# Performance work log

Hardware: AMD Instinct MI355X
Metric: run time of the kernel (lower is better)

Reference implementation:

```python
import jax, jax.numpy as jnp
import numpy as np

N = 40000      # nodes
E = 640000     # edges (avg degree 16)
D = 128        # feature dim (in_features == all hidden_dims due to residual)


def setup_inputs() -> dict:
    key = jax.random.key(0)
    ks = jax.random.split(key, 8)
    xavier = (6.0 / (D + D)) ** 0.5
    return {
        "x": jax.random.normal(ks[0], (N, D), dtype=jnp.float32),
        "edge_index": jax.random.randint(ks[1], (2, E), 0, N, dtype=jnp.int64),
        "W_t": jax.random.uniform(ks[2], (D, D), jnp.float32, -xavier, xavier),
        "b_t": jnp.zeros((D,), jnp.float32),
        "W0": jax.random.uniform(ks[3], (D, D), jnp.float32, -xavier, xavier),
        "b0": jnp.zeros((D,), jnp.float32),
        "W1": jax.random.uniform(ks[4], (D, D), jnp.float32, -xavier, xavier),
        "b1": jnp.zeros((D,), jnp.float32),
    }


def _gcn_layer(h, row, col, W, b):
    # linear transform, then edge-wise gather + scatter-add aggregation
    z = jnp.matmul(h, W)                                  # [N, D]
    agg = jnp.zeros_like(z).at[row].add(z[col])           # out[row] += z[col]
    return jax.nn.relu(agg + b)


def reference(x, edge_index, W_t, b_t, W0, b0, W1, b1):
    row, col = edge_index[0], edge_index[1]
    h = jnp.matmul(x, W_t) + b_t                          # self.transform
    # residual GCN layers (dropout p=0.0 -> identity; eval mode)
    h = h + _gcn_layer(h, row, col, W0, b0)
    h = h + _gcn_layer(h, row, col, W1, b1)
    return h
```

## Files before the change

### kernel.cpp

```cpp
#include <hip/hip_runtime.h>
#include <hip/hip_bf16.h>

#define N_NODES 40000
#define N_EDGES 640000
#define DIM     128
#define NB      157
#define GEMMB   625
#define HEB     1250

typedef __attribute__((ext_vector_type(8))) short short8;
typedef __attribute__((ext_vector_type(4))) float f32x4;

__device__ inline short f2bf(float f) {
    __hip_bfloat16 h = __float2bfloat16(f);
    return *reinterpret_cast<short*>(&h);
}
__device__ inline float bf2f(short u) {
    union { unsigned int i; float f; } x;
    x.i = ((unsigned int)(unsigned short)u) << 16;
    return x.f;
}

__device__ inline int fragidx(int k, int n) {
    int kb = k >> 5, kq = (k >> 3) & 3, j = k & 7;
    int nt = n >> 4, nl = n & 15;
    return (((kb * 8 + nt) * 64 + kq * 16 + nl) * 8 + j);
}

__global__ __launch_bounds__(256) void prep_zero(const float* __restrict__ Wt,
                                                 const float* __restrict__ W0,
                                                 const float* __restrict__ W1,
                                                 const float* __restrict__ bt,
                                                 short* __restrict__ WtF,
                                                 short* __restrict__ WfF,
                                                 short* __restrict__ W1F,
                                                 float* __restrict__ btf,
                                                 int* __restrict__ counts,
                                                 int* __restrict__ flagtot) {
    int b = blockIdx.x;
    if (b < 64) {
        int gid = b * 256 + threadIdx.x;
        int k = gid >> 7, n = gid & 127;
        float wf = 0.f;
        for (int kk = 0; kk < 128; ++kk)
            wf += Wt[k * 128 + kk] * W0[kk * 128 + n];
        int fi = fragidx(k, n);
        WtF[fi] = f2bf(Wt[k * 128 + n]);
        W1F[fi] = f2bf(W1[k * 128 + n]);
        WfF[fi] = f2bf(wf);
        if (gid < 128) {
            float s = 0.f;
            for (int kk = 0; kk < 128; ++kk) s += bt[kk] * W0[kk * 128 + n];
            btf[n] = s;
        }
    } else if (b < 64 + NB) {
        int i = (b - 64) * 256 + threadIdx.x;
        if (i < N_NODES) counts[i] = 0;
    } else {
        flagtot[threadIdx.x]       = 0;
        flagtot[threadIdx.x + 256] = 0;
    }
}

__global__ __launch_bounds__(256) void histrank_gemm(const int* __restrict__ rows,
                                                     int* __restrict__ counts,
                                                     unsigned short* __restrict__ rank,
                                                     const float* __restrict__ A,
                                                     const short* __restrict__ WtF,
                                                     const short* __restrict__ WfF,
                                                     const float* __restrict__ bt,
                                                     const float* __restrict__ btf,
                                                     float* __restrict__ H,
                                                     __hip_bfloat16* __restrict__ Z) {
    if (blockIdx.x < HEB) {
        int gid = blockIdx.x * 256 + threadIdx.x;
#pragma unroll
        for (int h = 0; h < 2; ++h) {
            int e = gid + h * HEB * 256;
            int r = rows[e];
            rank[e] = (unsigned short)atomicAdd(&counts[r], 1);
        }
        return;
    }

    const int t    = threadIdx.x;
    const int wave = t >> 6;
    const int l    = t & 63;
    const int nl   = l & 15;
    const int quad = l >> 4;
    const int wRow = (blockIdx.x - HEB) * 64 + wave * 16;

    f32x4 accH[8], accZ[8];
#pragma unroll
    for (int nt = 0; nt < 8; ++nt) {
        accH[nt] = (f32x4){0.f, 0.f, 0.f, 0.f};
        accZ[nt] = (f32x4){0.f, 0.f, 0.f, 0.f};
    }

#pragma unroll
    for (int kb = 0; kb < 4; ++kb) {
        const float* ap = A + (size_t)(wRow + nl) * 128 + kb * 32 + quad * 8;
        float4 f0 = *(const float4*)ap;
        float4 f1 = *(const float4*)(ap + 4);
        short8 afrag;
        afrag[0] = f2bf(f0.x); afrag[1] = f2bf(f0.y);
        afrag[2] = f2bf(f0.z); afrag[3] = f2bf(f0.w);
        afrag[4] = f2bf(f1.x); afrag[5] = f2bf(f1.y);
        afrag[6] = f2bf(f1.z); afrag[7] = f2bf(f1.w);
#pragma unroll
        for (int nt = 0; nt < 8; ++nt) {
            int off = ((kb * 8 + nt) * 64 + l) * 8;
            short8 bt_frag = *(const short8*)&WtF[off];
            short8 bf_frag = *(const short8*)&WfF[off];
            accH[nt] = __builtin_amdgcn_mfma_f32_16x16x32_bf16(afrag, bt_frag, accH[nt], 0, 0, 0);
            accZ[nt] = __builtin_amdgcn_mfma_f32_16x16x32_bf16(afrag, bf_frag, accZ[nt], 0, 0, 0);
        }
    }

#pragma unroll
    for (int nt = 0; nt < 8; ++nt) {
        int col = nt * 16 + nl;
        float bH = bt[col];
        float bZ = btf[col];
#pragma unroll
        for (int r = 0; r < 4; ++r) {
            int row = wRow + quad * 4 + r;
            H[(size_t)row * 128 + col] = accH[nt][r] + bH;
            *(short*)&Z[(size_t)row * 128 + col] = f2bf(accZ[nt][r] + bZ);
        }
    }
}

__global__ __launch_bounds__(256) void scan_onepass(const int* __restrict__ counts,
                                                    int* __restrict__ flags,
                                                    int* __restrict__ totals,
                                                    int* __restrict__ row_ptr) {
    __shared__ int sh[256];
    const int b = blockIdx.x;
    const int t = threadIdx.x;
    const int i = b * 256 + t;

    int c = (i < N_NODES) ? counts[i] : 0;
    int val = c;
    sh[t] = val;
    __syncthreads();
    for (int off = 1; off < 256; off <<= 1) {
        int a = (t >= off) ? sh[t - off] : 0;
        __syncthreads();
        val += a;
        sh[t] = val;
        __syncthreads();
    }
    const int excl  = val - c;
    const int total = sh[255];

    if (t == 0) {
        atomicExch(&totals[b], total);
        __threadfence();
        atomicExch(&flags[b], 1);
    }

    int v = 0;
    if (t < NB) {
        while (atomicAdd(&flags[t], 0) == 0) { }
        v = atomicAdd(&totals[t], 0);
    }
    __syncthreads();
    int val2 = v;
    sh[t] = val2;
    __syncthreads();
    for (int off = 1; off < 256; off <<= 1) {
        int a = (t >= off) ? sh[t - off] : 0;
        __syncthreads();
        val2 += a;
        sh[t] = val2;
        __syncthreads();
    }
    int blkOff = (b == 0) ? 0 : sh[b - 1];

    if (i < N_NODES) row_ptr[i] = excl + blkOff;
    if (i == 0) row_ptr[N_NODES] = N_EDGES;
}

__global__ __launch_bounds__(256) void scatter_plain(const int* __restrict__ rows,
                                                     const int* __restrict__ cols,
                                                     const unsigned short* __restrict__ rank,
                                                     const int* __restrict__ row_ptr,
                                                     unsigned short* __restrict__ adj) {
    int gid = blockIdx.x * 256 + threadIdx.x;
#pragma unroll
    for (int h = 0; h < 2; ++h) {
        int e = gid + h * HEB * 256;
        int r = rows[e];
        adj[row_ptr[r] + (int)rank[e]] = (unsigned short)cols[e];
    }
}

__global__ __launch_bounds__(256) void agg0_gemm(const __hip_bfloat16* __restrict__ z0,
                                                 const int* __restrict__ row_ptr,
                                                 const unsigned short* __restrict__ adj,
                                                 const float* __restrict__ bias,
                                                 const short* __restrict__ W1F,
                                                 float* __restrict__ H,
                                                 __hip_bfloat16* __restrict__ Z1) {
    __shared__ short hs[16][136];

    const int t    = threadIdx.x;
    const int wave = t >> 6;
    const int l    = t & 63;
    const int quad = l >> 4;
    const int sl   = l & 15;
    const int nodeBase = blockIdx.x * 16;

#pragma unroll
    for (int u = 0; u < 4; ++u) {
        const int m    = wave * 4 + u;
        const int node = nodeBase + m;
        const int s = row_ptr[node];
        const int e = row_ptr[node + 1];

        float acc[8];
#pragma unroll
        for (int j = 0; j < 8; ++j) acc[j] = 0.f;

        int it = s + quad;
        for (; it + 12 < e; it += 16) {
            int c0 = adj[it];
            int c1 = adj[it + 4];
            int c2 = adj[it + 8];
            int c3 = adj[it + 12];
            short8 v0 = *(const short8*)&z0[(size_t)c0 * DIM + sl * 8];
            short8 v1 = *(const short8*)&z0[(size_t)c1 * DIM + sl * 8];
            short8 v2 = *(const short8*)&z0[(size_t)c2 * DIM + sl * 8];
            short8 v3 = *(const short8*)&z0[(size_t)c3 * DIM + sl * 8];
#pragma unroll
            for (int j = 0; j < 8; ++j)
                acc[j] += (bf2f(v0[j]) + bf2f(v1[j])) + (bf2f(v2[j]) + bf2f(v3[j]));
        }
        for (; it + 4 < e; it += 8) {
            int c0 = adj[it];
            int c1 = adj[it + 4];
            short8 v0 = *(const short8*)&z0[(size_t)c0 * DIM + sl * 8];
            short8 v1 = *(const short8*)&z0[(size_t)c1 * DIM + sl * 8];
#pragma unroll
            for (int j = 0; j < 8; ++j) acc[j] += bf2f(v0[j]) + bf2f(v1[j]);
        }
        if (it < e) {
            int c = adj[it];
            short8 v = *(const short8*)&z0[(size_t)c * DIM + sl * 8];
#pragma unroll
            for (int j = 0; j < 8; ++j) acc[j] += bf2f(v[j]);
        }

#pragma unroll
        for (int j = 0; j < 8; ++j) acc[j] += __shfl_xor(acc[j], 16, 64);
#pragma unroll
        for (int j = 0; j < 8; ++j) acc[j] += __shfl_xor(acc[j], 32, 64);

        if (quad == 0) {
            float* hp = H + (size_t)node * DIM + sl * 8;
            float4 h0 = *(float4*)hp;
            float4 h1 = *(float4*)(hp + 4);
            float4 b0v = *(const float4*)&bias[sl * 8];
            float4 b1v = *(const float4*)&bias[sl * 8 + 4];
            float r[8];
            r[0] = acc[0] + b0v.x; r[1] = acc[1] + b0v.y; r[2] = acc[2] + b0v.z; r[3] = acc[3] + b0v.w;
            r[4] = acc[4] + b1v.x; r[5] = acc[5] + b1v.y; r[6] = acc[6] + b1v.z; r[7] = acc[7] + b1v.w;
            float hn[8];
            hn[0] = h0.x; hn[1] = h0.y; hn[2] = h0.z; hn[3] = h0.w;
            hn[4] = h1.x; hn[5] = h1.y; hn[6] = h1.z; hn[7] = h1.w;
            short8 o;
#pragma unroll
            for (int j = 0; j < 8; ++j) {
                float rr = r[j] > 0.f ? r[j] : 0.f;
                hn[j] += rr;
                o[j] = f2bf(hn[j]);
            }
            *(float4*)hp       = make_float4(hn[0], hn[1], hn[2], hn[3]);
            *(float4*)(hp + 4) = make_float4(hn[4], hn[5], hn[6], hn[7]);
            *(short8*)&hs[m][sl * 8] = o;
        }
    }
    __syncthreads();

    f32x4 acc2[2];
    acc2[0] = (f32x4){0.f, 0.f, 0.f, 0.f};
    acc2[1] = (f32x4){0.f, 0.f, 0.f, 0.f};
#pragma unroll
    for (int kb = 0; kb < 4; ++kb) {
        short8 afrag = *(const short8*)&hs[sl][kb * 32 + quad * 8];
#pragma unroll
        for (int nt2 = 0; nt2 < 2; ++nt2) {
            int nt = wave * 2 + nt2;
            short8 bfrag = *(const short8*)&W1F[((kb * 8 + nt) * 64 + l) * 8];
            acc2[nt2] = __builtin_amdgcn_mfma_f32_16x16x32_bf16(afrag, bfrag, acc2[nt2], 0, 0, 0);
        }
    }
#pragma unroll
    for (int nt2 = 0; nt2 < 2; ++nt2) {
        int col = (wave * 2 + nt2) * 16 + sl;
#pragma unroll
        for (int r = 0; r < 4; ++r) {
            int row = nodeBase + quad * 4 + r;
            *(short*)&Z1[(size_t)row * 128 + col] = f2bf(acc2[nt2][r]);
        }
    }
}

__global__ __launch_bounds__(256) void agg_final(const __hip_bfloat16* __restrict__ z,
                                                 const int* __restrict__ row_ptr,
                                                 const unsigned short* __restrict__ adj,
                                                 const float* __restrict__ bias,
                                                 float* __restrict__ H) {
    const int wave = threadIdx.x >> 6;
    const int l    = threadIdx.x & 63;
    const int quad = l >> 4;
    const int sl   = l & 15;
    const int node = blockIdx.x * 4 + wave;
    if (node >= N_NODES) return;

    const int s = row_ptr[node];
    const int e = row_ptr[node + 1];

    float acc[8];
#pragma unroll
    for (int j = 0; j < 8; ++j) acc[j] = 0.f;

    int it = s + quad;
    for (; it + 12 < e; it += 16) {
        int c0 = adj[it];
        int c1 = adj[it + 4];
        int c2 = adj[it + 8];
        int c3 = adj[it + 12];
        short8 v0 = *(const short8*)&z[(size_t)c0 * DIM + sl * 8];
        short8 v1 = *(const short8*)&z[(size_t)c1 * DIM + sl * 8];
        short8 v2 = *(const short8*)&z[(size_t)c2 * DIM + sl * 8];
        short8 v3 = *(const short8*)&z[(size_t)c3 * DIM + sl * 8];
#pragma unroll
        for (int j = 0; j < 8; ++j)
            acc[j] += (bf2f(v0[j]) + bf2f(v1[j])) + (bf2f(v2[j]) + bf2f(v3[j]));
    }
    for (; it + 4 < e; it += 8) {
        int c0 = adj[it];
        int c1 = adj[it + 4];
        short8 v0 = *(const short8*)&z[(size_t)c0 * DIM + sl * 8];
        short8 v1 = *(const short8*)&z[(size_t)c1 * DIM + sl * 8];
#pragma unroll
        for (int j = 0; j < 8; ++j) acc[j] += bf2f(v0[j]) + bf2f(v1[j]);
    }
    if (it < e) {
        int c = adj[it];
        short8 v = *(const short8*)&z[(size_t)c * DIM + sl * 8];
#pragma unroll
        for (int j = 0; j < 8; ++j) acc[j] += bf2f(v[j]);
    }

#pragma unroll
    for (int j = 0; j < 8; ++j) acc[j] += __shfl_xor(acc[j], 16, 64);
#pragma unroll
    for (int j = 0; j < 8; ++j) acc[j] += __shfl_xor(acc[j], 32, 64);

    if (quad == 0) {
        float* hp = H + (size_t)node * DIM + sl * 8;
        float4 h0 = *(float4*)hp;
        float4 h1 = *(float4*)(hp + 4);
        float4 b0 = *(const float4*)&bias[sl * 8];
        float4 b1 = *(const float4*)&bias[sl * 8 + 4];
        float r0 = acc[0] + b0.x, r1 = acc[1] + b0.y, r2 = acc[2] + b0.z, r3 = acc[3] + b0.w;
        float r4 = acc[4] + b1.x, r5 = acc[5] + b1.y, r6 = acc[6] + b1.z, r7 = acc[7] + b1.w;
        h0.x += r0 > 0.f ? r0 : 0.f;  h0.y += r1 > 0.f ? r1 : 0.f;
        h0.z += r2 > 0.f ? r2 : 0.f;  h0.w += r3 > 0.f ? r3 : 0.f;
        h1.x += r4 > 0.f ? r4 : 0.f;  h1.y += r5 > 0.f ? r5 : 0.f;
        h1.z += r6 > 0.f ? r6 : 0.f;  h1.w += r7 > 0.f ? r7 : 0.f;
        *(float4*)hp       = h0;
        *(float4*)(hp + 4) = h1;
    }
}

extern "C" void kernel_launch(void* const* d_in, const int* in_sizes, int n_in,
                              void* d_out, int out_size, void* d_ws, size_t ws_size,
                              hipStream_t stream) {
    const float* x   = (const float*)d_in[0];
    const int*   ei  = (const int*)d_in[1];
    const float* W_t = (const float*)d_in[2];
    const float* b_t = (const float*)d_in[3];
    const float* W0  = (const float*)d_in[4];
    const float* b0  = (const float*)d_in[5];
    const float* W1  = (const float*)d_in[6];
    const float* b1  = (const float*)d_in[7];

    const int* rows = ei;
    const int* cols = ei + N_EDGES;

    float* H = (float*)d_out;

    char* w = (char*)d_ws;
    __hip_bfloat16* Z0 = (__hip_bfloat16*)w;  w += (size_t)N_NODES * DIM * 2;
    __hip_bfloat16* Z1 = (__hip_bfloat16*)w;  w += (size_t)N_NODES * DIM * 2;
    short* WtF = (short*)w;  w += 128 * 128 * 2;
    short* WfF = (short*)w;  w += 128 * 128 * 2;
    short* W1F = (short*)w;  w += 128 * 128 * 2;
    float* btf = (float*)w;  w += 128 * 4;
    int* row_ptr = (int*)w;  w += (N_NODES + 1) * 4;
    int* counts  = (int*)w;  w += N_NODES * 4;
    int* flags   = (int*)w;  w += 256 * 4;
    int* totals  = (int*)w;  w += 256 * 4;
    unsigned short* rank = (unsigned short*)w;  w += (size_t)N_EDGES * 2;
    unsigned short* adj  = (unsigned short*)w;

    const int aggBlocks = (N_NODES + 3) / 4;

    prep_zero<<<64 + NB + 1, 256, 0, stream>>>(W_t, W0, W1, b_t, WtF, WfF, W1F,
                                               btf, counts, flags);

    histrank_gemm<<<HEB + GEMMB, 256, 0, stream>>>(rows, counts, rank,
                                                   x, WtF, WfF, b_t, btf, H, Z0);

    scan_onepass<<<NB, 256, 0, stream>>>(counts, flags, totals, row_ptr);

    scatter_plain<<<HEB, 256, 0, stream>>>(rows, cols, rank, row_ptr, adj);

    agg0_gemm<<<N_NODES / 16, 256, 0, stream>>>(Z0, row_ptr, adj, b0, W1F, H, Z1);

    agg_final<<<aggBlocks, 256, 0, stream>>>(Z1, row_ptr, adj, b1, H);
}
```

Measured before the change: 204.5 us.

## Replicate degree counters four ways and store second-layer features as fp8

The degree histogram is spread over four replicated counter arrays chosen by block index, which cuts atomic contention on hot rows. The scan sums the four copies and writes a per-replica absolute offset that the scatter uses. The second GCN layer's transformed features Z1 move from bf16 to fp8 (e4m3 via the packed conversion builtins), halving the bytes gathered in the final aggregation. The fp8 storage loses precision on activations and may break tolerance, and the replicas add extra zeroing and offset traffic.

```diff
diff --git a/kernel.cpp b/kernel.cpp
--- a/kernel.cpp
+++ b/kernel.cpp
@@ -7,9 +7,11 @@
 #define NB      157
 #define GEMMB   625
 #define HEB     1250
+#define NREP    4
 
 typedef __attribute__((ext_vector_type(8))) short short8;
 typedef __attribute__((ext_vector_type(4))) float f32x4;
+typedef __attribute__((ext_vector_type(2))) float f32x2;
 
 __device__ inline short f2bf(float f) {
     __hip_bfloat16 h = __float2bfloat16(f);
@@ -35,7 +37,7 @@
                                                  short* __restrict__ WfF,
                                                  short* __restrict__ W1F,
                                                  float* __restrict__ btf,
-                                                 int* __restrict__ counts,
+                                                 int* __restrict__ counts4,
                                                  int* __restrict__ flagtot) {
     int b = blockIdx.x;
     if (b < 64) {
@@ -53,9 +55,9 @@
             for (int kk = 0; kk < 128; ++kk) s += bt[kk] * W0[kk * 128 + n];
             btf[n] = s;
         }
-    } else if (b < 64 + NB) {
+    } else if (b < 64 + NREP * NB) {
         int i = (b - 64) * 256 + threadIdx.x;
-        if (i < N_NODES) counts[i] = 0;
+        if (i < NREP * N_NODES) counts4[i] = 0;
     } else {
         flagtot[threadIdx.x]       = 0;
         flagtot[threadIdx.x + 256] = 0;
@@ -63,7 +65,7 @@
 }
 
 __global__ __launch_bounds__(256) void histrank_gemm(const int* __restrict__ rows,
-                                                     int* __restrict__ counts,
+                                                     int* __restrict__ counts4,
                                                      unsigned short* __restrict__ rank,
                                                      const float* __restrict__ A,
                                                      const short* __restrict__ WtF,
@@ -74,11 +76,12 @@
                                                      __hip_bfloat16* __restrict__ Z) {
     if (blockIdx.x < HEB) {
         int gid = blockIdx.x * 256 + threadIdx.x;
+        int* cnt = counts4 + (blockIdx.x & (NREP - 1)) * N_NODES;
 #pragma unroll
         for (int h = 0; h < 2; ++h) {
             int e = gid + h * HEB * 256;
             int r = rows[e];
-            rank[e] = (unsigned short)atomicAdd(&counts[r], 1);
+            rank[e] = (unsigned short)atomicAdd(&cnt[r], 1);
         }
         return;
     }
@@ -131,16 +134,25 @@
     }
 }
 
-__global__ __launch_bounds__(256) void scan_onepass(const int* __restrict__ counts,
+__global__ __launch_bounds__(256) void scan_onepass(const int* __restrict__ counts4,
                                                     int* __restrict__ flags,
                                                     int* __restrict__ totals,
-                                                    int* __restrict__ row_ptr) {
+                                                    int* __restrict__ row_ptr,
+                                                    int* __restrict__ absOff) {
     __shared__ int sh[256];
     const int b = blockIdx.x;
     const int t = threadIdx.x;
     const int i = b * 256 + t;
 
-    int c = (i < N_NODES) ? counts[i] : 0;
+    int c0 = 0, c1 = 0, c2 = 0, c3 = 0;
+    if (i < N_NODES) {
+        c0 = counts4[0 * N_NODES + i];
+        c1 = counts4[1 * N_NODES + i];
+        c2 = counts4[2 * N_NODES + i];
+        c3 = counts4[3 * N_NODES + i];
+    }
+    const int c = c0 + c1 + c2 + c3;
+
     int val = c;
     sh[t] = val;
     __syncthreads();
@@ -178,21 +190,29 @@
     }
     int blkOff = (b == 0) ? 0 : sh[b - 1];
 
-    if (i < N_NODES) row_ptr[i] = excl + blkOff;
+    if (i < N_NODES) {
+        int base = excl + blkOff;
+        row_ptr[i] = base;
+        absOff[0 * N_NODES + i] = base;
+        absOff[1 * N_NODES + i] = base + c0;
+        absOff[2 * N_NODES + i] = base + c0 + c1;
+        absOff[3 * N_NODES + i] = base + c0 + c1 + c2;
+    }
     if (i == 0) row_ptr[N_NODES] = N_EDGES;
 }
 
 __global__ __launch_bounds__(256) void scatter_plain(const int* __restrict__ rows,
                                                      const int* __restrict__ cols,
                                                      const unsigned short* __restrict__ rank,
-                                                     const int* __restrict__ row_ptr,
+                                                     const int* __restrict__ absOff,
                                                      unsigned short* __restrict__ adj) {
     int gid = blockIdx.x * 256 + threadIdx.x;
+    const int* off = absOff + (blockIdx.x & (NREP - 1)) * N_NODES;
 #pragma unroll
     for (int h = 0; h < 2; ++h) {
         int e = gid + h * HEB * 256;
         int r = rows[e];
-        adj[row_ptr[r] + (int)rank[e]] = (unsigned short)cols[e];
+        adj[off[r] + (int)rank[e]] = (unsigned short)cols[e];
     }
 }
 
@@ -202,7 +222,7 @@
                                                  const float* __restrict__ bias,
                                                  const short* __restrict__ W1F,
                                                  float* __restrict__ H,
-                                                 __hip_bfloat16* __restrict__ Z1) {
+                                                 unsigned char* __restrict__ Z1) {
     __shared__ short hs[16][136];
 
     const int t    = threadIdx.x;
@@ -302,12 +322,14 @@
 #pragma unroll
         for (int r = 0; r < 4; ++r) {
             int row = nodeBase + quad * 4 + r;
-            *(short*)&Z1[(size_t)row * 128 + col] = f2bf(acc2[nt2][r]);
-        }
-    }
-}
-
-__global__ __launch_bounds__(256) void agg_final(const __hip_bfloat16* __restrict__ z,
+            float v = acc2[nt2][r];
+            int packed = __builtin_amdgcn_cvt_pk_fp8_f32(v, v, 0, false);
+            Z1[(size_t)row * 128 + col] = (unsigned char)(packed & 0xFF);
+        }
+    }
+}
+
+__global__ __launch_bounds__(256) void agg_final(const unsigned char* __restrict__ z1,
                                                  const int* __restrict__ row_ptr,
                                                  const unsigned short* __restrict__ adj,
                                                  const float* __restrict__ bias,
@@ -326,34 +348,41 @@
 #pragma unroll
     for (int j = 0; j < 8; ++j) acc[j] = 0.f;
 
+#define ADD_FP8(u2)                                                          \
+    {                                                                        \
+        f32x2 a0 = __builtin_amdgcn_cvt_pk_f32_fp8((u2).x, false);           \
+        f32x2 a1 = __builtin_amdgcn_cvt_pk_f32_fp8((u2).x, true);            \
+        f32x2 a2 = __builtin_amdgcn_cvt_pk_f32_fp8((u2).y, false);           \
+        f32x2 a3 = __builtin_amdgcn_cvt_pk_f32_fp8((u2).y, true);            \
+        acc[0] += a0.x; acc[1] += a0.y; acc[2] += a1.x; acc[3] += a1.y;      \
+        acc[4] += a2.x; acc[5] += a2.y; acc[6] += a3.x; acc[7] += a3.y;      \
+    }
+
     int it = s + quad;
     for (; it + 12 < e; it += 16) {
         int c0 = adj[it];
         int c1 = adj[it + 4];
         int c2 = adj[it + 8];
         int c3 = adj[it + 12];
-        short8 v0 = *(const short8*)&z[(size_t)c0 * DIM + sl * 8];
-        short8 v1 = *(const short8*)&z[(size_t)c1 * DIM + sl * 8];
-        short8 v2 = *(const short8*)&z[(size_t)c2 * DIM + sl * 8];
-        short8 v3 = *(const short8*)&z[(size_t)c3 * DIM + sl * 8];
-#pragma unroll
-        for (int j = 0; j < 8; ++j)
-            acc[j] += (bf2f(v0[j]) + bf2f(v1[j])) + (bf2f(v2[j]) + bf2f(v3[j]));
+        uint2 v0 = *(const uint2*)&z1[(size_t)c0 * 128 + sl * 8];
+        uint2 v1 = *(const uint2*)&z1[(size_t)c1 * 128 + sl * 8];
+        uint2 v2 = *(const uint2*)&z1[(size_t)c2 * 128 + sl * 8];
+        uint2 v3 = *(const uint2*)&z1[(size_t)c3 * 128 + sl * 8];
+        ADD_FP8(v0); ADD_FP8(v1); ADD_FP8(v2); ADD_FP8(v3);
     }
     for (; it + 4 < e; it += 8) {
         int c0 = adj[it];
         int c1 = adj[it + 4];
-        short8 v0 = *(const short8*)&z[(size_t)c0 * DIM + sl * 8];
-        short8 v1 = *(const short8*)&z[(size_t)c1 * DIM + sl * 8];
-#pragma unroll
-        for (int j = 0; j < 8; ++j) acc[j] += bf2f(v0[j]) + bf2f(v1[j]);
+        uint2 v0 = *(const uint2*)&z1[(size_t)c0 * 128 + sl * 8];
+        uint2 v1 = *(const uint2*)&z1[(size_t)c1 * 128 + sl * 8];
+        ADD_FP8(v0); ADD_FP8(v1);
     }
     if (it < e) {
         int c = adj[it];
-        short8 v = *(const short8*)&z[(size_t)c * DIM + sl * 8];
-#pragma unroll
-        for (int j = 0; j < 8; ++j) acc[j] += bf2f(v[j]);
-    }
+        uint2 v = *(const uint2*)&z1[(size_t)c * 128 + sl * 8];
+        ADD_FP8(v);
+    }
+#undef ADD_FP8
 
 #pragma unroll
     for (int j = 0; j < 8; ++j) acc[j] += __shfl_xor(acc[j], 16, 64);
@@ -396,13 +425,14 @@
 
     char* w = (char*)d_ws;
     __hip_bfloat16* Z0 = (__hip_bfloat16*)w;  w += (size_t)N_NODES * DIM * 2;
-    __hip_bfloat16* Z1 = (__hip_bfloat16*)w;  w += (size_t)N_NODES * DIM * 2;
+    unsigned char*  Z1 = (unsigned char*)w;   w += (size_t)N_NODES * DIM;
     short* WtF = (short*)w;  w += 128 * 128 * 2;
     short* WfF = (short*)w;  w += 128 * 128 * 2;
     short* W1F = (short*)w;  w += 128 * 128 * 2;
     float* btf = (float*)w;  w += 128 * 4;
     int* row_ptr = (int*)w;  w += (N_NODES + 1) * 4;
-    int* counts  = (int*)w;  w += N_NODES * 4;
+    int* counts4 = (int*)w;  w += NREP * N_NODES * 4;
+    int* absOff  = (int*)w;  w += NREP * N_NODES * 4;
     int* flags   = (int*)w;  w += 256 * 4;
     int* totals  = (int*)w;  w += 256 * 4;
     unsigned short* rank = (unsigned short*)w;  w += (size_t)N_EDGES * 2;
@@ -410,15 +440,15 @@
 
     const int aggBlocks = (N_NODES + 3) / 4;
 
-    prep_zero<<<64 + NB + 1, 256, 0, stream>>>(W_t, W0, W1, b_t, WtF, WfF, W1F,
-                                               btf, counts, flags);
-
-    histrank_gemm<<<HEB + GEMMB, 256, 0, stream>>>(rows, counts, rank,
+    prep_zero<<<64 + NREP * NB + 1, 256, 0, stream>>>(W_t, W0, W1, b_t, WtF, WfF,
+                                                      W1F, btf, counts4, flags);
+
+    histrank_gemm<<<HEB + GEMMB, 256, 0, stream>>>(rows, counts4, rank,
                                                    x, WtF, WfF, b_t, btf, H, Z0);
 
-    scan_onepass<<<NB, 256, 0, stream>>>(counts, flags, totals, row_ptr);
-
-    scatter_plain<<<HEB, 256, 0, stream>>>(rows, cols, rank, row_ptr, adj);
+    scan_onepass<<<NB, 256, 0, stream>>>(counts4, flags, totals, row_ptr, absOff);
+
+    scatter_plain<<<HEB, 256, 0, stream>>>(rows, cols, rank, absOff, adj);
 
     agg0_gemm<<<N_NODES / 16, 256, 0, stream>>>(Z0, row_ptr, adj, b0, W1F, H, Z1);
 
```

Result: faster. 199.4 us (-2.5%).
